# Kernel optimization log

Hardware: AMD Instinct MI355X
Metric: run time of the kernel (lower is better)

The kernel has to match this reference:

```python
import jax, jax.numpy as jnp
import numpy as np

N = 100000        # nodes
E = 1600000       # directed edges (avg degree 16)
F_IN, F_HID, F_OUT = 512, 32, 16


def setup_inputs() -> dict:
    key = jax.random.key(0)
    k0, k1, k2, k3 = jax.random.split(key, 4)
    x = jax.random.normal(k0, (N, F_IN), dtype=jnp.float32)
    edge_index = jax.random.randint(k1, (2, E), 0, N, dtype=jnp.int32)
    # Glorot-ish init for the two GCNConv linear weights
    W1 = jax.random.normal(k2, (F_IN, F_HID), dtype=jnp.float32) / np.float32(np.sqrt(F_IN))
    W2 = jax.random.normal(k3, (F_HID, F_OUT), dtype=jnp.float32) / np.float32(np.sqrt(F_HID))
    b1 = jnp.zeros((F_HID,), jnp.float32)
    b2 = jnp.zeros((F_OUT,), jnp.float32)
    return {"x": x, "W1": W1, "b1": b1, "W2": W2, "b2": b2, "edge_index": edge_index}


def gcn_conv(x, W, b, src, dst):
    """PyG GCNConv: h = x W; symmetric-normalized aggregation with self-loops; + bias."""
    h = x @ W                                   # [N, F_out] project first (PyG order)
    # degree including the implicit self-loop (start from ones)
    deg = jnp.ones((N,), h.dtype).at[dst].add(1.0)
    dinv = jax.lax.rsqrt(deg)                   # deg^{-1/2}
    coef = (dinv[src] * dinv[dst])[:, None]     # [E, 1] edge norm
    msg = h[src] * coef                         # gather + scale
    agg = jax.ops.segment_sum(msg, dst, num_segments=N)  # scatter-add to dst
    agg = agg + h * (dinv * dinv)[:, None]      # self-loop contribution
    return agg + b


def reference(x, W1, b1, W2, b2, edge_index):
    src, dst = edge_index[0], edge_index[1]
    h = jax.nn.relu(gcn_conv(x, W1, b1, src, dst))
    # F.dropout(training=self.training) is identity in eval mode
    h = gcn_conv(h, W2, b2, src, dst)
    return jax.nn.log_softmax(h, axis=1)
```

## Files before the change

kernel.cpp:

```cpp
#include <hip/hip_runtime.h>
#include <hip/hip_bf16.h>
#include <cstdint>

#define NN   100000
#define NE   1600000
#define FIN  512
#define FHID 32
#define FOUT 16

#define BSHIFT 8
#define BSIZE  256
#define NBUCK  391
#define HB     128
#define BEPB   4096
#define NBB    ((NE + BEPB - 1) / BEPB)
#define GB     3125

typedef float f32x4 __attribute__((ext_vector_type(4)));
typedef short s16x8 __attribute__((ext_vector_type(8)));
typedef short s16x4 __attribute__((ext_vector_type(4)));
typedef int   i32x4 __attribute__((ext_vector_type(4)));
typedef unsigned int u32;
typedef unsigned short u16;

__device__ __forceinline__ short f2bf(float f) {
  union { float f; uint32_t u; } v; v.f = f;
  uint32_t r = v.u + 0x7fffu + ((v.u >> 16) & 1u);
  return (short)(r >> 16);
}
__device__ __forceinline__ float bf2f(u16 u) {
  union { uint32_t u; float f; } v; v.u = (uint32_t)u << 16; return v.f;
}

__global__ __launch_bounds__(256) void k_hist(const int* __restrict__ dst,
                                              const float* __restrict__ W1,
                                              u16* __restrict__ wfrag,
                                              u32* __restrict__ bcount,
                                              u32* __restrict__ ticket,
                                              u32* __restrict__ bstart,
                                              u32* __restrict__ bcur) {
  __shared__ u32 h[NBUCK];
  __shared__ u32 wsum[4];
  __shared__ bool amlast;
  int tid = threadIdx.x;
  int lane = tid & 63;

  if (blockIdx.x == 0) {
    for (int it = 0; it < 64; ++it) {
      int flat = it * 256 + tid;
      int i  = flat & 7;
      int l  = (flat >> 3) & 63;
      int nt = (flat >> 9) & 1;
      int kt = flat >> 10;
      int k  = kt * 32 + ((l >> 4) << 3) + i;
      int n  = nt * 16 + (l & 15);
      wfrag[flat] = (u16)f2bf(W1[k * 32 + n]);
    }
  }

  for (int i = tid; i < NBUCK; i += 256) h[i] = 0;
  __syncthreads();
  const int stride = HB * 256 * 4;
  for (int e0 = (blockIdx.x * 256 + tid) * 4; e0 + 3 < NE; e0 += stride) {
    i32x4 d4 = *(const i32x4*)(dst + e0);
    atomicAdd(&h[d4[0] >> BSHIFT], 1u);
    atomicAdd(&h[d4[1] >> BSHIFT], 1u);
    atomicAdd(&h[d4[2] >> BSHIFT], 1u);
    atomicAdd(&h[d4[3] >> BSHIFT], 1u);
  }
  __syncthreads();
  for (int i = tid; i < NBUCK; i += 256)
    if (h[i]) atomicAdd(&bcount[i], h[i]);
  __syncthreads();
  if (tid == 0) {
    __threadfence();
    u32 t = __hip_atomic_fetch_add(ticket, 1u, __ATOMIC_ACQ_REL, __HIP_MEMORY_SCOPE_AGENT);
    amlast = (t == gridDim.x - 1);
  }
  __syncthreads();
  if (!amlast) return;

  u32 a0 = (2*tid   < NBUCK) ? __hip_atomic_load(&bcount[2*tid],   __ATOMIC_RELAXED, __HIP_MEMORY_SCOPE_AGENT) : 0;
  u32 a1 = (2*tid+1 < NBUCK) ? __hip_atomic_load(&bcount[2*tid+1], __ATOMIC_RELAXED, __HIP_MEMORY_SCOPE_AGENT) : 0;
  u32 s = a0 + a1;
  u32 v = s;
  #pragma unroll
  for (int off = 1; off < 64; off <<= 1) {
    u32 t = __shfl_up(v, off);
    if (lane >= off) v += t;
  }
  if (lane == 63) wsum[tid >> 6] = v;
  __syncthreads();
  if (tid < 4) {
    u32 w0 = wsum[tid], w = w0;
    #pragma unroll
    for (int off = 1; off < 4; off <<= 1) {
      u32 t = __shfl_up(w, off, 4);
      if ((tid & 3) >= off) w += t;
    }
    wsum[tid] = w - w0;
  }
  __syncthreads();
  u32 excl = v - s + wsum[tid >> 6];
  if (2*tid < NBUCK)   { bstart[2*tid]   = excl;      bcur[2*tid]   = excl; }
  if (2*tid+1 < NBUCK) { bstart[2*tid+1] = excl + a0; bcur[2*tid+1] = excl + a0; }
  if (tid == 255) bstart[NBUCK] = excl + s;
}

__global__ __launch_bounds__(512) void k_bin(const int* __restrict__ src,
                                             const int* __restrict__ dst,
                                             u32* __restrict__ bcur,
                                             u32* __restrict__ binned) {
  __shared__ u32 cnt[NBUCK];
  __shared__ u32 lofs[NBUCK];
  __shared__ u32 gbase[NBUCK];
  __shared__ u32 tmp[512];
  __shared__ u32 stage[BEPB];
  __shared__ u16 sb[BEPB];
  int tid = threadIdx.x;
  for (int i = tid; i < NBUCK; i += 512) cnt[i] = 0;
  __syncthreads();

  int base = blockIdx.x * BEPB;
  u32 vals[8]; u32 ofs[8]; int bks[8];
  #pragma unroll
  for (int half = 0; half < 2; ++half) {
    int e0 = base + tid * 8 + half * 4;
    if (e0 + 3 < NE) {
      i32x4 s4 = *(const i32x4*)(src + e0);
      i32x4 d4 = *(const i32x4*)(dst + e0);
      #pragma unroll
      for (int k = 0; k < 4; ++k) {
        int b = d4[k] >> BSHIFT;
        bks[half * 4 + k] = b;
        vals[half * 4 + k] = (u32)s4[k] | ((u32)(d4[k] & (BSIZE - 1)) << 17);
        ofs[half * 4 + k] = atomicAdd(&cnt[b], 1u);
      }
    } else {
      #pragma unroll
      for (int k = 0; k < 4; ++k) {
        int e = e0 + k;
        bool ok = e < NE;
        int s = 0, d = 0;
        if (ok) { s = src[e]; d = dst[e]; }
        int b = ok ? (d >> BSHIFT) : -1;
        bks[half * 4 + k] = b;
        vals[half * 4 + k] = (u32)s | ((u32)(d & (BSIZE - 1)) << 17);
        ofs[half * 4 + k] = ok ? atomicAdd(&cnt[b], 1u) : 0;
      }
    }
  }
  __syncthreads();

  u32 cv = (tid < NBUCK) ? cnt[tid] : 0;
  tmp[tid] = cv;
  __syncthreads();
  #pragma unroll
  for (int off = 1; off < 512; off <<= 1) {
    u32 t = (tid >= off) ? tmp[tid - off] : 0;
    __syncthreads();
    tmp[tid] += t;
    __syncthreads();
  }
  if (tid < NBUCK) {
    lofs[tid] = tmp[tid] - cv;
    gbase[tid] = cv ? atomicAdd(&bcur[tid], cv) : 0;
  }
  __syncthreads();
  u32 total = tmp[511];
  __syncthreads();

  #pragma unroll
  for (int k = 0; k < 8; ++k) {
    if (bks[k] >= 0) {
      u32 sl = lofs[bks[k]] + ofs[k];
      stage[sl] = vals[k];
      sb[sl] = (u16)bks[k];
    }
  }
  __syncthreads();

  for (u32 s2 = tid; s2 < total; s2 += 512) {
    int b = sb[s2];
    binned[gbase[b] + (s2 - lofs[b])] = stage[s2];
  }
}

__global__ __launch_bounds__(256) void k_fin(const u32* __restrict__ binned,
                                             const u32* __restrict__ bstart,
                                             int* __restrict__ deg,
                                             int* __restrict__ rs,
                                             float* __restrict__ dinv,
                                             int* __restrict__ csr) {
  __shared__ u32 degl[BSIZE];
  __shared__ u32 rsl[BSIZE];
  int tid = threadIdx.x;
  int b = blockIdx.x;
  u32 start = bstart[b];
  u32 n = bstart[b + 1] - start;

  degl[tid] = 0;
  __syncthreads();
  for (u32 k = tid; k < n; k += 256)
    atomicAdd(&degl[binned[start + k] >> 17], 1u);
  __syncthreads();

  u32 v = degl[tid];
  rsl[tid] = v;
  __syncthreads();
  #pragma unroll
  for (int off = 1; off < 256; off <<= 1) {
    u32 t = (tid >= off) ? rsl[tid - off] : 0;
    __syncthreads();
    rsl[tid] += t;
    __syncthreads();
  }
  u32 e = rsl[tid] - v;
  __syncthreads();
  rsl[tid] = e;

  int g = b * BSIZE + tid;
  if (g < NN) {
    deg[g] = (int)v;
    rs[g] = (int)(start + e);
    dinv[g] = rsqrtf(1.0f + (float)v);
  }
  __syncthreads();

  for (u32 k = tid; k < n; k += 256) {
    u32 vv = binned[start + k];
    u32 pos = atomicAdd(&rsl[vv >> 17], 1u);
    csr[start + pos] = (int)(vv & 0x1FFFFu);
  }
}

#define G1_ISSUE(TILE, HALF)                                                  \
  do {                                                                        \
    int r0_ = (TILE) * 16;                                                    \
    _Pragma("unroll")                                                         \
    for (int r_ = 0; r_ < 16; ++r_) {                                         \
      buf[r_] = *(const f32x4*)(x + (size_t)(r0_ + r_) * FIN +                \
                                (HALF) * 256 + lane * 4);                     \
    }                                                                         \
  } while (0)

#define G1_CVT(HALF)                                                          \
  do {                                                                        \
    _Pragma("unroll")                                                         \
    for (int r_ = 0; r_ < 16; ++r_) {                                         \
      u32 sw_ = (u32)((r_ & 7) << 4);                                         \
      s16x4 w_;                                                               \
      _Pragma("unroll")                                                       \
      for (int q_ = 0; q_ < 4; ++q_) w_[q_] = f2bf(buf[r_][q_]);              \
      *(s16x4*)(xw + (((u32)(r_ * 1024 + (HALF) * 512 + lane * 8)) ^ sw_)) = w_; \
    }                                                                         \
  } while (0)

#define G1_MFMAH(HALF)                                                        \
  do {                                                                        \
    _Pragma("unroll")                                                         \
    for (int kt_ = (HALF) * 8; kt_ < (HALF) * 8 + 8; ++kt_) {                 \
      s16x8 af_ = *(const s16x8*)(xw +                                        \
          (((u32)(m * 1024 + kt_ * 64 + h * 16)) ^ msw));                     \
      s16x8 b0_ = wf[(kt_ * 2 + 0) * 64 + lane];                              \
      s16x8 b1_ = wf[(kt_ * 2 + 1) * 64 + lane];                              \
      acc0 = __builtin_amdgcn_mfma_f32_16x16x32_bf16(af_, b0_, acc0, 0,0,0);  \
      acc1 = __builtin_amdgcn_mfma_f32_16x16x32_bf16(af_, b1_, acc1, 0,0,0);  \
    }                                                                         \
  } while (0)

#define G1_STORE(TILE)                                                        \
  do {                                                                        \
    int r0_ = (TILE) * 16;                                                    \
    _Pragma("unroll")                                                         \
    for (int r_ = 0; r_ < 4; ++r_) {                                          \
      int row_ = r0_ + h * 4 + r_;                                            \
      float di_ = dinv[row_];                                                 \
      u16* o_ = Hs1 + (size_t)row_ * FHID + m;                                \
      o_[0]  = (u16)f2bf(acc0[r_] * di_);                                     \
      o_[16] = (u16)f2bf(acc1[r_] * di_);                                     \
    }                                                                         \
  } while (0)

__global__ __launch_bounds__(64) void k_gemm1(const float* __restrict__ x,
                                              const u16* __restrict__ wfrag,
                                              const float* __restrict__ dinv,
                                              u16* __restrict__ Hs1) {
  __shared__ u16 Xs[16][512];
  const int lane = threadIdx.x;
  char* xw = (char*)Xs;
  const int h = lane >> 4;
  const int m = lane & 15;
  const u32 msw = (u32)((m & 7) << 4);
  const s16x8* wf = (const s16x8*)wfrag;
  const int t0 = blockIdx.x * 2;

  f32x4 buf[16];
  f32x4 acc0, acc1;

  G1_ISSUE(t0, 0);   G1_CVT(0);
  G1_ISSUE(t0, 1);   acc0 = (f32x4){}; acc1 = (f32x4){};
                     G1_MFMAH(0);  G1_CVT(1);
  G1_ISSUE(t0+1, 0); G1_MFMAH(1);  G1_STORE(t0);  G1_CVT(0);
  G1_ISSUE(t0+1, 1); acc0 = (f32x4){}; acc1 = (f32x4){};
                     G1_MFMAH(0);  G1_CVT(1);
                     G1_MFMAH(1);  G1_STORE(t0+1);
}

__global__ __launch_bounds__(256) void k_gat1(const int* __restrict__ csr,
                                              const int* __restrict__ rs,
                                              const int* __restrict__ deg,
                                              const float* __restrict__ dinv,
                                              const float* __restrict__ b1,
                                              const float* __restrict__ W2,
                                              const u16* __restrict__ Hs1,
                                              u16* __restrict__ Hs2) {
  __shared__ float w[FHID * FOUT];
  for (int i = threadIdx.x; i < FHID * FOUT; i += 256) w[i] = W2[i];
  __syncthreads();

  int t = blockIdx.x * 256 + threadIdx.x;
  int d = t >> 2;
  if (d >= NN) return;
  int p = t & 3;
  int start = rs[d], n = deg[d];

  float a0[8], a1[8], a2[8], a3[8];
  {
    s16x8 v = *(const s16x8*)(Hs1 + (size_t)d * FHID + p * 8);
    #pragma unroll
    for (int k = 0; k < 8; ++k) {
      a0[k] = bf2f((u16)v[k]); a1[k] = 0.f; a2[k] = 0.f; a3[k] = 0.f;
    }
  }
  int j = 0;
  for (; j + 8 <= n; j += 8) {
    int s0=csr[start+j],   s1=csr[start+j+1], s2=csr[start+j+2], s3=csr[start+j+3];
    int s4=csr[start+j+4], s5=csr[start+j+5], s6=csr[start+j+6], s7=csr[start+j+7];
    s16x8 v0 = *(const s16x8*)(Hs1 + (size_t)s0 * FHID + p * 8);
    s16x8 v1 = *(const s16x8*)(Hs1 + (size_t)s1 * FHID + p * 8);
    s16x8 v2 = *(const s16x8*)(Hs1 + (size_t)s2 * FHID + p * 8);
    s16x8 v3 = *(const s16x8*)(Hs1 + (size_t)s3 * FHID + p * 8);
    s16x8 v4 = *(const s16x8*)(Hs1 + (size_t)s4 * FHID + p * 8);
    s16x8 v5 = *(const s16x8*)(Hs1 + (size_t)s5 * FHID + p * 8);
    s16x8 v6 = *(const s16x8*)(Hs1 + (size_t)s6 * FHID + p * 8);
    s16x8 v7 = *(const s16x8*)(Hs1 + (size_t)s7 * FHID + p * 8);
    #pragma unroll
    for (int k = 0; k < 8; ++k) {
      a0[k] += bf2f((u16)v0[k]);
      a1[k] += bf2f((u16)v1[k]);
      a2[k] += bf2f((u16)v2[k]);
      a3[k] += bf2f((u16)v3[k]);
      a0[k] += bf2f((u16)v4[k]);
      a1[k] += bf2f((u16)v5[k]);
      a2[k] += bf2f((u16)v6[k]);
      a3[k] += bf2f((u16)v7[k]);
    }
  }
  for (; j + 4 <= n; j += 4) {
    int s0=csr[start+j], s1=csr[start+j+1], s2=csr[start+j+2], s3=csr[start+j+3];
    s16x8 v0 = *(const s16x8*)(Hs1 + (size_t)s0 * FHID + p * 8);
    s16x8 v1 = *(const s16x8*)(Hs1 + (size_t)s1 * FHID + p * 8);
    s16x8 v2 = *(const s16x8*)(Hs1 + (size_t)s2 * FHID + p * 8);
    s16x8 v3 = *(const s16x8*)(Hs1 + (size_t)s3 * FHID + p * 8);
    #pragma unroll
    for (int k = 0; k < 8; ++k) {
      a0[k] += bf2f((u16)v0[k]);
      a1[k] += bf2f((u16)v1[k]);
      a2[k] += bf2f((u16)v2[k]);
      a3[k] += bf2f((u16)v3[k]);
    }
  }
  for (; j < n; ++j) {
    int s0 = csr[start + j];
    s16x8 v0 = *(const s16x8*)(Hs1 + (size_t)s0 * FHID + p * 8);
    #pragma unroll
    for (int k = 0; k < 8; ++k) a0[k] += bf2f((u16)v0[k]);
  }

  float dd = dinv[d];
  float h[8];
  #pragma unroll
  for (int k = 0; k < 8; ++k)
    h[k] = fmaxf(((a0[k] + a1[k]) + (a2[k] + a3[k])) * dd + b1[p * 8 + k], 0.0f);

  float pj[FOUT];
  #pragma unroll
  for (int jj = 0; jj < FOUT; ++jj) pj[jj] = 0.f;
  #pragma unroll
  for (int k = 0; k < 8; ++k)
    #pragma unroll
    for (int jj = 0; jj < FOUT; ++jj)
      pj[jj] = fmaf(h[k], w[(p * 8 + k) * FOUT + jj], pj[jj]);
  #pragma unroll
  for (int jj = 0; jj < FOUT; ++jj) {
    pj[jj] += __shfl_xor(pj[jj], 1);
    pj[jj] += __shfl_xor(pj[jj], 2);
  }
  s16x4 o;
  #pragma unroll
  for (int q = 0; q < 4; ++q) o[q] = f2bf(pj[p * 4 + q] * dd);
  *(s16x4*)(Hs2 + (size_t)d * FOUT + p * 4) = o;
}

__global__ __launch_bounds__(256) void k_gat2(const int* __restrict__ csr,
                                              const int* __restrict__ rs,
                                              const int* __restrict__ deg,
                                              const float* __restrict__ dinv,
                                              const float* __restrict__ b2,
                                              const u16* __restrict__ Hs2,
                                              float* __restrict__ out) {
  int t = blockIdx.x * 256 + threadIdx.x;
  int d = t >> 2;
  if (d >= NN) return;
  int p = t & 3;
  int start = rs[d], n = deg[d];

  float a0[4], a1[4], a2[4], a3[4];
  {
    s16x4 v = *(const s16x4*)(Hs2 + (size_t)d * FOUT + p * 4);
    #pragma unroll
    for (int k = 0; k < 4; ++k) { a0[k] = bf2f((u16)v[k]); a1[k]=0.f; a2[k]=0.f; a3[k]=0.f; }
  }
  int j = 0;
  for (; j + 8 <= n; j += 8) {
    int s0=csr[start+j],   s1=csr[start+j+1], s2=csr[start+j+2], s3=csr[start+j+3];
    int s4=csr[start+j+4], s5=csr[start+j+5], s6=csr[start+j+6], s7=csr[start+j+7];
    s16x4 v0 = *(const s16x4*)(Hs2 + (size_t)s0 * FOUT + p * 4);
    s16x4 v1 = *(const s16x4*)(Hs2 + (size_t)s1 * FOUT + p * 4);
    s16x4 v2 = *(const s16x4*)(Hs2 + (size_t)s2 * FOUT + p * 4);
    s16x4 v3 = *(const s16x4*)(Hs2 + (size_t)s3 * FOUT + p * 4);
    s16x4 v4 = *(const s16x4*)(Hs2 + (size_t)s4 * FOUT + p * 4);
    s16x4 v5 = *(const s16x4*)(Hs2 + (size_t)s5 * FOUT + p * 4);
    s16x4 v6 = *(const s16x4*)(Hs2 + (size_t)s6 * FOUT + p * 4);
    s16x4 v7 = *(const s16x4*)(Hs2 + (size_t)s7 * FOUT + p * 4);
    #pragma unroll
    for (int k = 0; k < 4; ++k) {
      a0[k] += bf2f((u16)v0[k]); a1[k] += bf2f((u16)v1[k]);
      a2[k] += bf2f((u16)v2[k]); a3[k] += bf2f((u16)v3[k]);
      a0[k] += bf2f((u16)v4[k]); a1[k] += bf2f((u16)v5[k]);
      a2[k] += bf2f((u16)v6[k]); a3[k] += bf2f((u16)v7[k]);
    }
  }
  for (; j + 4 <= n; j += 4) {
    int s0=csr[start+j], s1=csr[start+j+1], s2=csr[start+j+2], s3=csr[start+j+3];
    s16x4 v0 = *(const s16x4*)(Hs2 + (size_t)s0 * FOUT + p * 4);
    s16x4 v1 = *(const s16x4*)(Hs2 + (size_t)s1 * FOUT + p * 4);
    s16x4 v2 = *(const s16x4*)(Hs2 + (size_t)s2 * FOUT + p * 4);
    s16x4 v3 = *(const s16x4*)(Hs2 + (size_t)s3 * FOUT + p * 4);
    #pragma unroll
    for (int k = 0; k < 4; ++k) {
      a0[k] += bf2f((u16)v0[k]); a1[k] += bf2f((u16)v1[k]);
      a2[k] += bf2f((u16)v2[k]); a3[k] += bf2f((u16)v3[k]);
    }
  }
  for (; j < n; ++j) {
    int s0 = csr[start + j];
    s16x4 v0 = *(const s16x4*)(Hs2 + (size_t)s0 * FOUT + p * 4);
    #pragma unroll
    for (int k = 0; k < 4; ++k) a0[k] += bf2f((u16)v0[k]);
  }

  float dd = dinv[d];
  float z[4];
  #pragma unroll
  for (int k = 0; k < 4; ++k)
    z[k] = ((a0[k]+a1[k]) + (a2[k]+a3[k])) * dd + b2[p * 4 + k];

  float m = fmaxf(fmaxf(z[0], z[1]), fmaxf(z[2], z[3]));
  m = fmaxf(m, __shfl_xor(m, 1));
  m = fmaxf(m, __shfl_xor(m, 2));
  float s = expf(z[0]-m) + expf(z[1]-m) + expf(z[2]-m) + expf(z[3]-m);
  s += __shfl_xor(s, 1);
  s += __shfl_xor(s, 2);
  float lse = m + logf(s);

  f32x4 o = { z[0]-lse, z[1]-lse, z[2]-lse, z[3]-lse };
  *(f32x4*)(out + (size_t)d * FOUT + p * 4) = o;
}

extern "C" void kernel_launch(void* const* d_in, const int* in_sizes, int n_in,
                              void* d_out, int out_size, void* d_ws, size_t ws_size,
                              hipStream_t stream) {
  const float* x  = (const float*)d_in[0];
  const float* W1 = (const float*)d_in[1];
  const float* b1 = (const float*)d_in[2];
  const float* W2 = (const float*)d_in[3];
  const float* b2 = (const float*)d_in[4];
  const int*   ei = (const int*)d_in[5];
  const int* srcv = ei;
  const int* dstv = ei + NE;

  char* ws = (char*)d_ws;
  const size_t KB = 1024, MB = 1048576;
  u32*   bcount = (u32*)(ws + 0);
  u32*   ticket = (u32*)(ws + 1600);
  u32*   bstart = (u32*)(ws + 8 * KB);
  u32*   bcur   = (u32*)(ws + 16 * KB);
  u16*   wfrag  = (u16*)(ws + 64 * KB);
  int*   deg    = (int*)(ws + 512 * KB);
  int*   rs     = (int*)(ws + 1024 * KB);
  float* dinv   = (float*)(ws + 1536 * KB);
  u32*   binned = (u32*)(ws + 2 * MB);
  int*   csr    = (int*)(ws + 9 * MB);
  u16*   Hs1    = (u16*)(ws + 16 * MB);
  u16*   Hs2    = (u16*)(ws + 23 * MB);
  float* out    = (float*)d_out;

  hipMemsetAsync(ws, 0, 2 * KB, stream);

  k_hist <<<HB,   256, 0, stream>>>(dstv, W1, wfrag, bcount, ticket, bstart, bcur);
  k_bin  <<<NBB,  512, 0, stream>>>(srcv, dstv, bcur, binned);
  k_fin  <<<NBUCK, 256, 0, stream>>>(binned, bstart, deg, rs, dinv, csr);
  k_gemm1<<<GB, 64, 0, stream>>>(x, wfrag, dinv, Hs1);
  k_gat1 <<<(NN * 4 + 255) / 256, 256, 0, stream>>>(csr, rs, deg, dinv, b1, W2, Hs1, Hs2);
  k_gat2 <<<(NN * 4 + 255) / 256, 256, 0, stream>>>(csr, rs, deg, dinv, b2, Hs2, out);
}
```

Baseline: 134.6 us.

## Process four row tiles per GEMM1 block and prefetch CSR indices in gathers

The first-layer GEMM kernel now handles four 16-row tiles per block instead of two. It extends the software pipeline across tiles and clamps or guards rows past the node count. Both gather kernels now load the next group of eight CSR neighbor indices while the current feature rows are being fetched, to hide index-load latency. The 4-wide remainder loop is removed, so up to seven leftover edges go through the scalar tail, and the larger GEMM blocks halve the grid size.

New measurement: 137.6 us. 1.02x slower.

```diff
diff --git a/kernel.cpp b/kernel.cpp
--- a/kernel.cpp
+++ b/kernel.cpp
@@ -14,7 +14,8 @@
 #define HB     128
 #define BEPB   4096
 #define NBB    ((NE + BEPB - 1) / BEPB)
-#define GB     3125
+#define NTILE  6250
+#define GB     ((NTILE + 3) / 4)
 
 typedef float f32x4 __attribute__((ext_vector_type(4)));
 typedef short s16x8 __attribute__((ext_vector_type(8)));
@@ -239,7 +240,9 @@
     int r0_ = (TILE) * 16;                                                    \
     _Pragma("unroll")                                                         \
     for (int r_ = 0; r_ < 16; ++r_) {                                         \
-      buf[r_] = *(const f32x4*)(x + (size_t)(r0_ + r_) * FIN +                \
+      int row_ = r0_ + r_;                                                    \
+      if (row_ >= NN) row_ = NN - 1;                                          \
+      buf[r_] = *(const f32x4*)(x + (size_t)row_ * FIN +                      \
                                 (HALF) * 256 + lane * 4);                     \
     }                                                                         \
   } while (0)
@@ -275,10 +278,12 @@
     _Pragma("unroll")                                                         \
     for (int r_ = 0; r_ < 4; ++r_) {                                          \
       int row_ = r0_ + h * 4 + r_;                                            \
-      float di_ = dinv[row_];                                                 \
-      u16* o_ = Hs1 + (size_t)row_ * FHID + m;                                \
-      o_[0]  = (u16)f2bf(acc0[r_] * di_);                                     \
-      o_[16] = (u16)f2bf(acc1[r_] * di_);                                     \
+      if (row_ < NN) {                                                        \
+        float di_ = dinv[row_];                                               \
+        u16* o_ = Hs1 + (size_t)row_ * FHID + m;                              \
+        o_[0]  = (u16)f2bf(acc0[r_] * di_);                                   \
+        o_[16] = (u16)f2bf(acc1[r_] * di_);                                   \
+      }                                                                       \
     }                                                                         \
   } while (0)
 
@@ -293,7 +298,7 @@
   const int m = lane & 15;
   const u32 msw = (u32)((m & 7) << 4);
   const s16x8* wf = (const s16x8*)wfrag;
-  const int t0 = blockIdx.x * 2;
+  const int t0 = blockIdx.x * 4;
 
   f32x4 buf[16];
   f32x4 acc0, acc1;
@@ -301,10 +306,13 @@
   G1_ISSUE(t0, 0);   G1_CVT(0);
   G1_ISSUE(t0, 1);   acc0 = (f32x4){}; acc1 = (f32x4){};
                      G1_MFMAH(0);  G1_CVT(1);
-  G1_ISSUE(t0+1, 0); G1_MFMAH(1);  G1_STORE(t0);  G1_CVT(0);
-  G1_ISSUE(t0+1, 1); acc0 = (f32x4){}; acc1 = (f32x4){};
-                     G1_MFMAH(0);  G1_CVT(1);
-                     G1_MFMAH(1);  G1_STORE(t0+1);
+  #pragma unroll
+  for (int i = 0; i < 3; ++i) {
+    G1_ISSUE(t0+i+1, 0); G1_MFMAH(1);  G1_STORE(t0+i);  G1_CVT(0);
+    G1_ISSUE(t0+i+1, 1); acc0 = (f32x4){}; acc1 = (f32x4){};
+                         G1_MFMAH(0);  G1_CVT(1);
+  }
+  G1_MFMAH(1);  G1_STORE(t0+3);
 }
 
 __global__ __launch_bounds__(256) void k_gat1(const int* __restrict__ csr,
@@ -334,41 +342,32 @@
     }
   }
   int j = 0;
-  for (; j + 8 <= n; j += 8) {
-    int s0=csr[start+j],   s1=csr[start+j+1], s2=csr[start+j+2], s3=csr[start+j+3];
-    int s4=csr[start+j+4], s5=csr[start+j+5], s6=csr[start+j+6], s7=csr[start+j+7];
-    s16x8 v0 = *(const s16x8*)(Hs1 + (size_t)s0 * FHID + p * 8);
-    s16x8 v1 = *(const s16x8*)(Hs1 + (size_t)s1 * FHID + p * 8);
-    s16x8 v2 = *(const s16x8*)(Hs1 + (size_t)s2 * FHID + p * 8);
-    s16x8 v3 = *(const s16x8*)(Hs1 + (size_t)s3 * FHID + p * 8);
-    s16x8 v4 = *(const s16x8*)(Hs1 + (size_t)s4 * FHID + p * 8);
-    s16x8 v5 = *(const s16x8*)(Hs1 + (size_t)s5 * FHID + p * 8);
-    s16x8 v6 = *(const s16x8*)(Hs1 + (size_t)s6 * FHID + p * 8);
-    s16x8 v7 = *(const s16x8*)(Hs1 + (size_t)s7 * FHID + p * 8);
-    #pragma unroll
-    for (int k = 0; k < 8; ++k) {
-      a0[k] += bf2f((u16)v0[k]);
-      a1[k] += bf2f((u16)v1[k]);
-      a2[k] += bf2f((u16)v2[k]);
-      a3[k] += bf2f((u16)v3[k]);
-      a0[k] += bf2f((u16)v4[k]);
-      a1[k] += bf2f((u16)v5[k]);
-      a2[k] += bf2f((u16)v6[k]);
-      a3[k] += bf2f((u16)v7[k]);
-    }
-  }
-  for (; j + 4 <= n; j += 4) {
-    int s0=csr[start+j], s1=csr[start+j+1], s2=csr[start+j+2], s3=csr[start+j+3];
-    s16x8 v0 = *(const s16x8*)(Hs1 + (size_t)s0 * FHID + p * 8);
-    s16x8 v1 = *(const s16x8*)(Hs1 + (size_t)s1 * FHID + p * 8);
-    s16x8 v2 = *(const s16x8*)(Hs1 + (size_t)s2 * FHID + p * 8);
-    s16x8 v3 = *(const s16x8*)(Hs1 + (size_t)s3 * FHID + p * 8);
-    #pragma unroll
-    for (int k = 0; k < 8; ++k) {
-      a0[k] += bf2f((u16)v0[k]);
-      a1[k] += bf2f((u16)v1[k]);
-      a2[k] += bf2f((u16)v2[k]);
-      a3[k] += bf2f((u16)v3[k]);
+  if (n >= 8) {
+    int c0=csr[start],   c1=csr[start+1], c2=csr[start+2], c3=csr[start+3];
+    int c4=csr[start+4], c5=csr[start+5], c6=csr[start+6], c7=csr[start+7];
+    for (; j + 8 <= n; j += 8) {
+      s16x8 v0 = *(const s16x8*)(Hs1 + (size_t)c0 * FHID + p * 8);
+      s16x8 v1 = *(const s16x8*)(Hs1 + (size_t)c1 * FHID + p * 8);
+      s16x8 v2 = *(const s16x8*)(Hs1 + (size_t)c2 * FHID + p * 8);
+      s16x8 v3 = *(const s16x8*)(Hs1 + (size_t)c3 * FHID + p * 8);
+      s16x8 v4 = *(const s16x8*)(Hs1 + (size_t)c4 * FHID + p * 8);
+      s16x8 v5 = *(const s16x8*)(Hs1 + (size_t)c5 * FHID + p * 8);
+      s16x8 v6 = *(const s16x8*)(Hs1 + (size_t)c6 * FHID + p * 8);
+      s16x8 v7 = *(const s16x8*)(Hs1 + (size_t)c7 * FHID + p * 8);
+      int nb = start + (((j + 16) <= n) ? (j + 8) : (n - 8));
+      c0 = csr[nb];     c1 = csr[nb + 1]; c2 = csr[nb + 2]; c3 = csr[nb + 3];
+      c4 = csr[nb + 4]; c5 = csr[nb + 5]; c6 = csr[nb + 6]; c7 = csr[nb + 7];
+      #pragma unroll
+      for (int k = 0; k < 8; ++k) {
+        a0[k] += bf2f((u16)v0[k]);
+        a1[k] += bf2f((u16)v1[k]);
+        a2[k] += bf2f((u16)v2[k]);
+        a3[k] += bf2f((u16)v3[k]);
+        a0[k] += bf2f((u16)v4[k]);
+        a1[k] += bf2f((u16)v5[k]);
+        a2[k] += bf2f((u16)v6[k]);
+        a3[k] += bf2f((u16)v7[k]);
+      }
     }
   }
   for (; j < n; ++j) {
@@ -423,35 +422,28 @@
     for (int k = 0; k < 4; ++k) { a0[k] = bf2f((u16)v[k]); a1[k]=0.f; a2[k]=0.f; a3[k]=0.f; }
   }
   int j = 0;
-  for (; j + 8 <= n; j += 8) {
-    int s0=csr[start+j],   s1=csr[start+j+1], s2=csr[start+j+2], s3=csr[start+j+3];
-    int s4=csr[start+j+4], s5=csr[start+j+5], s6=csr[start+j+6], s7=csr[start+j+7];
-    s16x4 v0 = *(const s16x4*)(Hs2 + (size_t)s0 * FOUT + p * 4);
-    s16x4 v1 = *(const s16x4*)(Hs2 + (size_t)s1 * FOUT + p * 4);
-    s16x4 v2 = *(const s16x4*)(Hs2 + (size_t)s2 * FOUT + p * 4);
-    s16x4 v3 = *(const s16x4*)(Hs2 + (size_t)s3 * FOUT + p * 4);
-    s16x4 v4 = *(const s16x4*)(Hs2 + (size_t)s4 * FOUT + p * 4);
-    s16x4 v5 = *(const s16x4*)(Hs2 + (size_t)s5 * FOUT + p * 4);
-    s16x4 v6 = *(const s16x4*)(Hs2 + (size_t)s6 * FOUT + p * 4);
-    s16x4 v7 = *(const s16x4*)(Hs2 + (size_t)s7 * FOUT + p * 4);
-    #pragma unroll
-    for (int k = 0; k < 4; ++k) {
-      a0[k] += bf2f((u16)v0[k]); a1[k] += bf2f((u16)v1[k]);
-      a2[k] += bf2f((u16)v2[k]); a3[k] += bf2f((u16)v3[k]);
-      a0[k] += bf2f((u16)v4[k]); a1[k] += bf2f((u16)v5[k]);
-      a2[k] += bf2f((u16)v6[k]); a3[k] += bf2f((u16)v7[k]);
-    }
-  }
-  for (; j + 4 <= n; j += 4) {
-    int s0=csr[start+j], s1=csr[start+j+1], s2=csr[start+j+2], s3=csr[start+j+3];
-    s16x4 v0 = *(const s16x4*)(Hs2 + (size_t)s0 * FOUT + p * 4);
-    s16x4 v1 = *(const s16x4*)(Hs2 + (size_t)s1 * FOUT + p * 4);
-    s16x4 v2 = *(const s16x4*)(Hs2 + (size_t)s2 * FOUT + p * 4);
-    s16x4 v3 = *(const s16x4*)(Hs2 + (size_t)s3 * FOUT + p * 4);
-    #pragma unroll
-    for (int k = 0; k < 4; ++k) {
-      a0[k] += bf2f((u16)v0[k]); a1[k] += bf2f((u16)v1[k]);
-      a2[k] += bf2f((u16)v2[k]); a3[k] += bf2f((u16)v3[k]);
+  if (n >= 8) {
+    int c0=csr[start],   c1=csr[start+1], c2=csr[start+2], c3=csr[start+3];
+    int c4=csr[start+4], c5=csr[start+5], c6=csr[start+6], c7=csr[start+7];
+    for (; j + 8 <= n; j += 8) {
+      s16x4 v0 = *(const s16x4*)(Hs2 + (size_t)c0 * FOUT + p * 4);
+      s16x4 v1 = *(const s16x4*)(Hs2 + (size_t)c1 * FOUT + p * 4);
+      s16x4 v2 = *(const s16x4*)(Hs2 + (size_t)c2 * FOUT + p * 4);
+      s16x4 v3 = *(const s16x4*)(Hs2 + (size_t)c3 * FOUT + p * 4);
+      s16x4 v4 = *(const s16x4*)(Hs2 + (size_t)c4 * FOUT + p * 4);
+      s16x4 v5 = *(const s16x4*)(Hs2 + (size_t)c5 * FOUT + p * 4);
+      s16x4 v6 = *(const s16x4*)(Hs2 + (size_t)c6 * FOUT + p * 4);
+      s16x4 v7 = *(const s16x4*)(Hs2 + (size_t)c7 * FOUT + p * 4);
+      int nb = start + (((j + 16) <= n) ? (j + 8) : (n - 8));
+      c0 = csr[nb];     c1 = csr[nb + 1]; c2 = csr[nb + 2]; c3 = csr[nb + 3];
+      c4 = csr[nb + 4]; c5 = csr[nb + 5]; c6 = csr[nb + 6]; c7 = csr[nb + 7];
+      #pragma unroll
+      for (int k = 0; k < 4; ++k) {
+        a0[k] += bf2f((u16)v0[k]); a1[k] += bf2f((u16)v1[k]);
+        a2[k] += bf2f((u16)v2[k]); a3[k] += bf2f((u16)v3[k]);
+        a0[k] += bf2f((u16)v4[k]); a1[k] += bf2f((u16)v5[k]);
+        a2[k] += bf2f((u16)v6[k]); a3[k] += bf2f((u16)v7[k]);
+      }
     }
   }
   for (; j < n; ++j) {
```
